# Performance work log

Measured on AMD Instinct MI355X. Metric: run time of the kernel, lower is better.

The kernel has to match this reference:

```python
import jax, jax.numpy as jnp
import numpy as np

IN_FEAT, H_FEAT, NUM_CLASSES = 7, 8, 2
N_NODES, N_EDGES, N_GRAPHS = 40000, 640000, 64
DIMS = [IN_FEAT, H_FEAT, H_FEAT * 2, H_FEAT * 4, H_FEAT * 8, H_FEAT * 16]  # 7,8,16,32,64,128


def setup_inputs() -> dict:
    key = jax.random.key(0)
    ks = jax.random.split(key, 20)
    inp = {
        "x": jax.random.normal(ks[0], (N_NODES, IN_FEAT), dtype=jnp.float32),
        "edge_index": jax.random.randint(ks[1], (2, N_EDGES), 0, N_NODES, dtype=jnp.int32),
        "edge_attr": jax.random.uniform(ks[2], (N_EDGES,), dtype=jnp.float32),
        "batch": jnp.sort(jax.random.randint(ks[3], (N_NODES,), 0, N_GRAPHS, dtype=jnp.int32)),
    }
    # GraphConv params: lin_rel (with bias) applied to aggregated messages,
    # lin_root (no bias) applied to x itself. Stored as [in, out]; y = x @ W.
    for i in range(5):
        fi, fo = DIMS[i], DIMS[i + 1]
        s = 1.0 / np.sqrt(fi)
        inp[f"w_rel{i+1}"] = jax.random.uniform(ks[4 + 3 * i], (fi, fo), minval=-s, maxval=s, dtype=jnp.float32)
        inp[f"b_rel{i+1}"] = jax.random.uniform(ks[5 + 3 * i], (fo,), minval=-s, maxval=s, dtype=jnp.float32)
        inp[f"w_root{i+1}"] = jax.random.uniform(ks[6 + 3 * i], (fi, fo), minval=-s, maxval=s, dtype=jnp.float32)
    s = 1.0 / np.sqrt(DIMS[-1])
    inp["w_lin"] = jax.random.uniform(ks[19], (DIMS[-1], NUM_CLASSES), minval=-s, maxval=s, dtype=jnp.float32)
    inp["b_lin"] = jax.random.uniform(jax.random.fold_in(key, 99), (NUM_CLASSES,), minval=-s, maxval=s, dtype=jnp.float32)
    return inp


def graph_conv(x, src, dst, ew, w_rel, b_rel, w_root):
    # message: edge_weight * x[src]; aggregate by sum at dst (PyG GraphConv, aggr='add')
    msg = x[src] * ew[:, None]                               # [E, Fin]
    agg = jax.ops.segment_sum(msg, dst, num_segments=N_NODES)  # [N, Fin]
    return agg @ w_rel + b_rel + x @ w_root                  # [N, Fout]


def reference(x, edge_index, edge_attr, batch,
              w_rel1, b_rel1, w_root1, w_rel2, b_rel2, w_root2,
              w_rel3, b_rel3, w_root3, w_rel4, b_rel4, w_root4,
              w_rel5, b_rel5, w_root5, w_lin, b_lin):
    src, dst = edge_index[0], edge_index[1]
    h = x
    params = [(w_rel1, b_rel1, w_root1), (w_rel2, b_rel2, w_root2),
              (w_rel3, b_rel3, w_root3), (w_rel4, b_rel4, w_root4),
              (w_rel5, b_rel5, w_root5)]
    for wr, br, wo in params:
        h = graph_conv(h, src, dst, edge_attr, wr, br, wo)
    pooled = jax.ops.segment_sum(h, batch, num_segments=N_GRAPHS)  # [G, 128]
    return pooled @ w_lin + b_lin                                  # [G, 2]
```

## Files before the change

### kernel.cpp

```cpp
#include <hip/hip_runtime.h>

#define N_NODES 40000
#define N_EDGES 640000
#define N_GRAPHS 64

typedef unsigned short u16;
typedef unsigned int u32;
typedef __attribute__((ext_vector_type(8))) short bf16x8;
typedef __attribute__((ext_vector_type(4))) float f32x4;

static inline int cdiv(long long a, int b) { return (int)((a + b - 1) / b); }

__device__ __forceinline__ u16 f2bf(float f) {
    u32 u = __float_as_uint(f);
    u32 r = (u + 0x7fffu + ((u >> 16) & 1u)) >> 16;
    return (u16)r;
}
__device__ __forceinline__ u32 packpair(float a, float b) {
    return (u32)f2bf(a) | ((u32)f2bf(b) << 16);
}
__device__ __forceinline__ void unpack8(uint4 q, float* o) {
    o[0] = __uint_as_float(q.x << 16); o[1] = __uint_as_float(q.x & 0xffff0000u);
    o[2] = __uint_as_float(q.y << 16); o[3] = __uint_as_float(q.y & 0xffff0000u);
    o[4] = __uint_as_float(q.z << 16); o[5] = __uint_as_float(q.z & 0xffff0000u);
    o[6] = __uint_as_float(q.w << 16); o[7] = __uint_as_float(q.w & 0xffff0000u);
}

__device__ __forceinline__ void pack_one(int idx, int KS, int Kreal, int FOUT,
                                         const float* __restrict__ wrel,
                                         const float* __restrict__ wroot,
                                         u16* __restrict__ out) {
    int j = idx & 7;
    int lane = (idx >> 3) & 63;
    int rest = idx >> 9;
    int nt = rest / KS, ks = rest - nt * KS;
    int k = ks * 32 + (lane >> 4) * 8 + j;
    int col = nt * 16 + (lane & 15);
    float v = 0.f;
    if (k < Kreal / 2) v = wrel[k * FOUT + col];
    else if (k < Kreal) v = wroot[(k - Kreal / 2) * FOUT + col];
    out[idx] = f2bf(v);
}

__global__ __launch_bounds__(256) void prep_kernel(
        const float* __restrict__ x, u16* __restrict__ xbf,
        const float* __restrict__ wr2, const float* __restrict__ wo2,
        const float* __restrict__ wr3, const float* __restrict__ wo3,
        const float* __restrict__ wr4, const float* __restrict__ wo4,
        const float* __restrict__ wr5, const float* __restrict__ wo5,
        u16* __restrict__ p2, u16* __restrict__ p3,
        u16* __restrict__ p4, u16* __restrict__ p5,
        int* __restrict__ deg, float* __restrict__ pooled) {
    int tid = blockIdx.x * 256 + threadIdx.x;
    if (tid < 40000) {
        int n = tid;
        float v[8];
        #pragma unroll
        for (int i = 0; i < 7; ++i) v[i] = x[n * 7 + i];
        v[7] = 0.f;
        uint4 q;
        q.x = packpair(v[0], v[1]); q.y = packpair(v[2], v[3]);
        q.z = packpair(v[4], v[5]); q.w = packpair(v[6], v[7]);
        *(uint4*)(xbf + (long long)n * 8) = q;
    } else if (tid < 62016) {
        int t = tid - 40000;
        if (t < 512)        pack_one(t,        1,  16,  16,  wr2, wo2, p2);
        else if (t < 1536)  pack_one(t - 512,  1,  32,  32,  wr3, wo3, p3);
        else if (t < 5632)  pack_one(t - 1536, 2,  64,  64,  wr4, wo4, p4);
        else                pack_one(t - 5632, 4, 128, 128,  wr5, wo5, p5);
    } else if (tid < 102016) {
        deg[tid - 62016] = 0;
    } else if (tid < 110208) {
        pooled[tid - 102016] = 0.f;
    }
}

__global__ __launch_bounds__(256) void hist_kernel(const int* __restrict__ dst,
                                                   int* __restrict__ deg) {
    int e = blockIdx.x * 256 + threadIdx.x;
    if (e < N_EDGES) atomicAdd(&deg[dst[e]], 1);
}

__global__ __launch_bounds__(1024) void scan_part(const int* __restrict__ deg,
                                                  int* __restrict__ row_start,
                                                  int* __restrict__ bsum) {
    __shared__ int wtot[16], woff[16];
    int tid = threadIdx.x;
    int i = blockIdx.x * 1024 + tid;
    int v = (i < N_NODES) ? deg[i] : 0;
    int lane = tid & 63, wid = tid >> 6;
    int inc = v;
    #pragma unroll
    for (int off = 1; off < 64; off <<= 1) {
        int y = __shfl_up(inc, off, 64);
        if (lane >= off) inc += y;
    }
    if (lane == 63) wtot[wid] = inc;
    __syncthreads();
    if (tid < 16) {
        int b = wtot[tid];
        #pragma unroll
        for (int off = 1; off < 16; off <<= 1) {
            int y = __shfl_up(b, off, 16);
            if ((tid & 15) >= off) b += y;
        }
        woff[tid] = b - wtot[tid];
        if (tid == 15) bsum[blockIdx.x] = b;
    }
    __syncthreads();
    if (i <= N_NODES) row_start[i] = woff[wid] + inc - v;
}

__global__ __launch_bounds__(1024) void scan_add(int* __restrict__ row_start,
                                                 const int* __restrict__ bsum,
                                                 int* __restrict__ cursor) {
    __shared__ int sbase;
    int tid = threadIdx.x;
    if (tid < 64) {
        int b = (tid < blockIdx.x) ? bsum[tid] : 0;
        #pragma unroll
        for (int off = 32; off; off >>= 1) b += __shfl_xor(b, off, 64);
        if (tid == 0) sbase = b;
    }
    __syncthreads();
    int i = blockIdx.x * 1024 + tid;
    if (i <= N_NODES) {
        int v = row_start[i] + sbase;
        row_start[i] = v;
        if (i < N_NODES) cursor[i] = v;
    }
}

__global__ __launch_bounds__(256) void scatter_kernel(const int* __restrict__ src,
                                                      const int* __restrict__ dst,
                                                      const float* __restrict__ ew,
                                                      int* __restrict__ cursor,
                                                      int2* __restrict__ csr_pair) {
    int e = blockIdx.x * 256 + threadIdx.x;
    if (e >= N_EDGES) return;
    int pos = atomicAdd(&cursor[dst[e]], 1);
    int2 q;
    q.x = src[e];
    q.y = __float_as_int(ew[e]);
    csr_pair[pos] = q;
}

template<int LOGF, int SLOG>
__global__ __launch_bounds__(256) void gather_bf16(const u16* __restrict__ hin,
                                                   const int* __restrict__ rs,
                                                   const int2* __restrict__ pair,
                                                   u16* __restrict__ agg) {
    constexpr int FIN = 8 << LOGF;
    constexpr int S = 1 << SLOG;
    long long tid = (long long)blockIdx.x * 256 + threadIdx.x;
    int n = (int)(tid >> (LOGF + SLOG));
    if (n >= N_NODES) return;
    int sub = (int)(tid & ((1 << (LOGF + SLOG)) - 1));
    int c = sub & ((1 << LOGF) - 1);
    int half = sub >> LOGF;
    const u16* base = hin + c * 8;
    int beg = rs[n], end = rs[n + 1];
    float acc[8] = {0.f, 0.f, 0.f, 0.f, 0.f, 0.f, 0.f, 0.f};
    int p = beg + half;
    int s = 0; float w = 0.f;
    if (p < end) { int2 q = pair[p]; s = q.x; w = __int_as_float(q.y); }
    while (p < end) {
        uint4 rq = *(const uint4*)(base + (long long)s * FIN);
        float wc = w;
        int pn = p + S;
        if (pn < end) { int2 q = pair[pn]; s = q.x; w = __int_as_float(q.y); }
        float tv[8];
        unpack8(rq, tv);
        #pragma unroll
        for (int j = 0; j < 8; ++j) acc[j] = fmaf(wc, tv[j], acc[j]);
        p = pn;
    }
    #pragma unroll
    for (int d = (1 << LOGF); d < (1 << (LOGF + SLOG)); d <<= 1) {
        #pragma unroll
        for (int j = 0; j < 8; ++j) acc[j] += __shfl_xor(acc[j], d, 64);
    }
    if (half == 0) {
        uint4 o;
        o.x = packpair(acc[0], acc[1]); o.y = packpair(acc[2], acc[3]);
        o.z = packpair(acc[4], acc[5]); o.w = packpair(acc[6], acc[7]);
        *(uint4*)(agg + (long long)n * FIN + c * 8) = o;
    }
}

__global__ __launch_bounds__(256) void node1b(const u16* __restrict__ agg1,
                                              const u16* __restrict__ xbf,
                                              const float* __restrict__ wr,
                                              const float* __restrict__ br,
                                              const float* __restrict__ wo,
                                              u16* __restrict__ h2) {
    __shared__ float swr[56], swo[56], sb[8];
    if (threadIdx.x < 56) { swr[threadIdx.x] = wr[threadIdx.x]; swo[threadIdx.x] = wo[threadIdx.x]; }
    if (threadIdx.x < 8) sb[threadIdx.x] = br[threadIdx.x];
    __syncthreads();
    int n = blockIdx.x * 256 + threadIdx.x;
    if (n >= N_NODES) return;
    float a[8], h[8];
    uint4 qa = *(const uint4*)(agg1 + (long long)n * 8);
    uint4 qh = *(const uint4*)(xbf + (long long)n * 8);
    unpack8(qa, a);
    unpack8(qh, h);
    float o[8];
    #pragma unroll
    for (int j = 0; j < 8; ++j) {
        float s = sb[j];
        #pragma unroll
        for (int i = 0; i < 7; ++i) s = fmaf(a[i], swr[i * 8 + j], fmaf(h[i], swo[i * 8 + j], s));
        o[j] = s;
    }
    uint4 q;
    q.x = packpair(o[0], o[1]); q.y = packpair(o[2], o[3]);
    q.z = packpair(o[4], o[5]); q.w = packpair(o[6], o[7]);
    *(uint4*)(h2 + (long long)n * 8) = q;
}

template<int FIN, int FOUT, bool POOL>
__global__ __launch_bounds__(64) void node_mfma(const u16* __restrict__ agg,
                                                const u16* __restrict__ hin,
                                                const u16* __restrict__ bpack,
                                                const float* __restrict__ b_rel,
                                                u16* __restrict__ hout,
                                                const int* __restrict__ batch,
                                                float* __restrict__ pooled) {
    constexpr int KREAL = 2 * FIN;
    constexpr int K = (KREAL < 32) ? 32 : KREAL;
    constexpr int KS = K / 32;
    constexpr int NT = FOUT / 16;
    int lane = threadIdx.x;
    int tile = blockIdx.x;
    int col = lane & 15;
    int node_a = tile * 16 + col;
    int kgrp = (lane >> 4) * 8;

    f32x4 acc[NT];
    #pragma unroll
    for (int nt = 0; nt < NT; ++nt) {
        float bv = b_rel[nt * 16 + col];
        acc[nt] = (f32x4){bv, bv, bv, bv};
    }

    #pragma unroll
    for (int ks = 0; ks < KS; ++ks) {
        int k0 = ks * 32 + kgrp;
        bf16x8 af;
        if (k0 < FIN)
            af = *(const bf16x8*)(agg + (long long)node_a * FIN + k0);
        else if (k0 < KREAL)
            af = *(const bf16x8*)(hin + (long long)node_a * FIN + (k0 - FIN));
        else
            af = (bf16x8)(short)0;
        #pragma unroll
        for (int nt = 0; nt < NT; ++nt) {
            bf16x8 bf = *(const bf16x8*)(bpack + (((nt * KS + ks) << 6) + lane) * 8);
            acc[nt] = __builtin_amdgcn_mfma_f32_16x16x32_bf16(af, bf, acc[nt], 0, 0, 0);
        }
    }

    int row0 = tile * 16 + (lane >> 4) * 4;
    if constexpr (!POOL) {
        #pragma unroll
        for (int nt = 0; nt < NT; ++nt)
            #pragma unroll
            for (int r = 0; r < 4; ++r)
                hout[(long long)(row0 + r) * FOUT + nt * 16 + col] = f2bf(acc[nt][r]);
    } else {
        int b_first = batch[tile * 16];
        int b_last = batch[tile * 16 + 15];
        if (b_first == b_last) {
            #pragma unroll
            for (int nt = 0; nt < NT; ++nt) {
                float s = acc[nt][0] + acc[nt][1] + acc[nt][2] + acc[nt][3];
                s += __shfl_xor(s, 16, 64);
                s += __shfl_xor(s, 32, 64);
                if (lane < 16) atomicAdd(&pooled[b_first * FOUT + nt * 16 + col], s);
            }
        } else {
            #pragma unroll
            for (int r = 0; r < 4; ++r) {
                int g = batch[row0 + r];
                #pragma unroll
                for (int nt = 0; nt < NT; ++nt)
                    atomicAdd(&pooled[g * FOUT + nt * 16 + col], acc[nt][r]);
            }
        }
    }
}

__global__ void final_kernel(const float* __restrict__ pooled,
                             const float* __restrict__ w_lin,
                             const float* __restrict__ b_lin,
                             float* __restrict__ out) {
    int tid = threadIdx.x;
    int g = tid >> 1;
    int c = tid & 1;
    float acc = b_lin[c];
    #pragma unroll 8
    for (int fi = 0; fi < 128; ++fi)
        acc += pooled[g * 128 + fi] * w_lin[fi * 2 + c];
    out[g * 2 + c] = acc;
}

extern "C" void kernel_launch(void* const* d_in, const int* in_sizes, int n_in,
                              void* d_out, int out_size, void* d_ws, size_t ws_size,
                              hipStream_t stream) {
    const float* x     = (const float*)d_in[0];
    const int*   ei    = (const int*)d_in[1];
    const float* ea    = (const float*)d_in[2];
    const int*   batch = (const int*)d_in[3];
    const int* src = ei;
    const int* dst = ei + N_EDGES;

    const float* w_rel[5], *b_rel[5], *w_root[5];
    for (int i = 0; i < 5; ++i) {
        w_rel[i]  = (const float*)d_in[4 + 3 * i];
        b_rel[i]  = (const float*)d_in[5 + 3 * i];
        w_root[i] = (const float*)d_in[6 + 3 * i];
    }
    const float* w_lin = (const float*)d_in[19];
    const float* b_lin = (const float*)d_in[20];
    float* out = (float*)d_out;

    u16*   xbf     = (u16*)d_ws;
    u16*   agg     = xbf + 320000;
    u16*   h2      = agg + 2560000;
    u16*   h3      = h2 + 320000;
    u16*   h4      = h3 + 640000;
    u16*   h5      = h4 + 1280000;
    float* pooled  = (float*)(h5 + 2560000);
    u16*   p2      = (u16*)(pooled + N_GRAPHS * 128);
    u16*   p3      = p2 + 512;
    u16*   p4      = p3 + 1024;
    u16*   p5      = p4 + 4096;
    int2*  csr_pair= (int2*)(p5 + 16384);
    int*   deg     = (int*)(csr_pair + N_EDGES);
    int*   rs      = deg + N_NODES;
    int*   cursor  = rs + N_NODES + 1;
    int*   bsum    = cursor + N_NODES;

    const int BLK = 256;
    const int EB = cdiv(N_EDGES, BLK);

    prep_kernel<<<431, BLK, 0, stream>>>(x, xbf,
                                         w_rel[1], w_root[1], w_rel[2], w_root[2],
                                         w_rel[3], w_root[3], w_rel[4], w_root[4],
                                         p2, p3, p4, p5, deg, pooled);
    hist_kernel<<<EB, BLK, 0, stream>>>(dst, deg);
    scan_part<<<40, 1024, 0, stream>>>(deg, rs, bsum);
    scan_add<<<40, 1024, 0, stream>>>(rs, bsum, cursor);
    scatter_kernel<<<EB, BLK, 0, stream>>>(src, dst, ea, cursor, csr_pair);

    gather_bf16<0, 3><<<cdiv((long long)N_NODES * 8, BLK), BLK, 0, stream>>>(
        xbf, rs, csr_pair, agg);
    node1b<<<cdiv(N_NODES, BLK), BLK, 0, stream>>>(agg, xbf, w_rel[0], b_rel[0], w_root[0], h2);

    gather_bf16<0, 3><<<cdiv((long long)N_NODES * 8, BLK), BLK, 0, stream>>>(
        h2, rs, csr_pair, agg);
    node_mfma<8, 16, false><<<2500, 64, 0, stream>>>(agg, h2, p2, b_rel[1], h3, nullptr, nullptr);

    gather_bf16<1, 3><<<cdiv((long long)N_NODES * 16, BLK), BLK, 0, stream>>>(
        h3, rs, csr_pair, agg);
    node_mfma<16, 32, false><<<2500, 64, 0, stream>>>(agg, h3, p3, b_rel[2], h4, nullptr, nullptr);

    gather_bf16<2, 3><<<cdiv((long long)N_NODES * 32, BLK), BLK, 0, stream>>>(
        h4, rs, csr_pair, agg);
    node_mfma<32, 64, false><<<2500, 64, 0, stream>>>(agg, h4, p4, b_rel[3], h5, nullptr, nullptr);

    gather_bf16<3, 3><<<cdiv((long long)N_NODES * 64, BLK), BLK, 0, stream>>>(
        h5, rs, csr_pair, agg);
    node_mfma<64, 128, true><<<2500, 64, 0, stream>>>(agg, h5, p5, b_rel[4], nullptr, batch, pooled);

    final_kernel<<<1, 128, 0, stream>>>(pooled, w_lin, b_lin, out);
}
```

Measured before the change: 240.8 us.

## Fuse neighbor gather with dense transform per layer via LDS staging

Merges each layer's CSR gather into the MFMA node-transform kernel, staging the 16-node aggregate tile in shared memory instead of writing and rereading a global agg buffer. Layer 1's gather is also fused with its scalar transform, with each of 8 lanes producing one output feature. This removes kernel launches and global traffic for the aggregate. The cost is 1024-thread blocks with one wave per node, which leaves many lanes idle for narrow layers, and only NT waves doing MFMA after the barrier.

```diff
diff --git a/kernel.cpp b/kernel.cpp
--- a/kernel.cpp
+++ b/kernel.cpp
@@ -145,29 +145,30 @@
     csr_pair[pos] = q;
 }
 
-template<int LOGF, int SLOG>
-__global__ __launch_bounds__(256) void gather_bf16(const u16* __restrict__ hin,
-                                                   const int* __restrict__ rs,
-                                                   const int2* __restrict__ pair,
-                                                   u16* __restrict__ agg) {
-    constexpr int FIN = 8 << LOGF;
-    constexpr int S = 1 << SLOG;
-    long long tid = (long long)blockIdx.x * 256 + threadIdx.x;
-    int n = (int)(tid >> (LOGF + SLOG));
+__global__ __launch_bounds__(256) void gather_node1(const u16* __restrict__ xbf,
+                                                    const int* __restrict__ rs,
+                                                    const int2* __restrict__ pair,
+                                                    const float* __restrict__ wr,
+                                                    const float* __restrict__ br,
+                                                    const float* __restrict__ wo,
+                                                    u16* __restrict__ h2) {
+    __shared__ float swr[56], swo[56], sb[8];
+    if (threadIdx.x < 56) { swr[threadIdx.x] = wr[threadIdx.x]; swo[threadIdx.x] = wo[threadIdx.x]; }
+    if (threadIdx.x < 8) sb[threadIdx.x] = br[threadIdx.x];
+    __syncthreads();
+    int tid = blockIdx.x * 256 + threadIdx.x;
+    int n = tid >> 3;
     if (n >= N_NODES) return;
-    int sub = (int)(tid & ((1 << (LOGF + SLOG)) - 1));
-    int c = sub & ((1 << LOGF) - 1);
-    int half = sub >> LOGF;
-    const u16* base = hin + c * 8;
+    int s3 = tid & 7;
     int beg = rs[n], end = rs[n + 1];
     float acc[8] = {0.f, 0.f, 0.f, 0.f, 0.f, 0.f, 0.f, 0.f};
-    int p = beg + half;
+    int p = beg + s3;
     int s = 0; float w = 0.f;
     if (p < end) { int2 q = pair[p]; s = q.x; w = __int_as_float(q.y); }
     while (p < end) {
-        uint4 rq = *(const uint4*)(base + (long long)s * FIN);
+        uint4 rq = *(const uint4*)(xbf + (long long)s * 8);
         float wc = w;
-        int pn = p + S;
+        int pn = p + 8;
         if (pn < end) { int2 q = pair[pn]; s = q.x; w = __int_as_float(q.y); }
         float tv[8];
         unpack8(rq, tv);
@@ -176,116 +177,119 @@
         p = pn;
     }
     #pragma unroll
-    for (int d = (1 << LOGF); d < (1 << (LOGF + SLOG)); d <<= 1) {
+    for (int d = 1; d < 8; d <<= 1) {
         #pragma unroll
         for (int j = 0; j < 8; ++j) acc[j] += __shfl_xor(acc[j], d, 64);
     }
-    if (half == 0) {
-        uint4 o;
-        o.x = packpair(acc[0], acc[1]); o.y = packpair(acc[2], acc[3]);
-        o.z = packpair(acc[4], acc[5]); o.w = packpair(acc[6], acc[7]);
-        *(uint4*)(agg + (long long)n * FIN + c * 8) = o;
-    }
-}
-
-__global__ __launch_bounds__(256) void node1b(const u16* __restrict__ agg1,
-                                              const u16* __restrict__ xbf,
-                                              const float* __restrict__ wr,
-                                              const float* __restrict__ br,
-                                              const float* __restrict__ wo,
-                                              u16* __restrict__ h2) {
-    __shared__ float swr[56], swo[56], sb[8];
-    if (threadIdx.x < 56) { swr[threadIdx.x] = wr[threadIdx.x]; swo[threadIdx.x] = wo[threadIdx.x]; }
-    if (threadIdx.x < 8) sb[threadIdx.x] = br[threadIdx.x];
-    __syncthreads();
-    int n = blockIdx.x * 256 + threadIdx.x;
-    if (n >= N_NODES) return;
-    float a[8], h[8];
-    uint4 qa = *(const uint4*)(agg1 + (long long)n * 8);
     uint4 qh = *(const uint4*)(xbf + (long long)n * 8);
-    unpack8(qa, a);
+    float h[8];
     unpack8(qh, h);
-    float o[8];
+    float o = sb[s3];
     #pragma unroll
-    for (int j = 0; j < 8; ++j) {
-        float s = sb[j];
-        #pragma unroll
-        for (int i = 0; i < 7; ++i) s = fmaf(a[i], swr[i * 8 + j], fmaf(h[i], swo[i * 8 + j], s));
-        o[j] = s;
-    }
-    uint4 q;
-    q.x = packpair(o[0], o[1]); q.y = packpair(o[2], o[3]);
-    q.z = packpair(o[4], o[5]); q.w = packpair(o[6], o[7]);
-    *(uint4*)(h2 + (long long)n * 8) = q;
-}
-
-template<int FIN, int FOUT, bool POOL>
-__global__ __launch_bounds__(64) void node_mfma(const u16* __restrict__ agg,
-                                                const u16* __restrict__ hin,
-                                                const u16* __restrict__ bpack,
-                                                const float* __restrict__ b_rel,
-                                                u16* __restrict__ hout,
-                                                const int* __restrict__ batch,
-                                                float* __restrict__ pooled) {
+    for (int i = 0; i < 7; ++i)
+        o = fmaf(acc[i], swr[i * 8 + s3], fmaf(h[i], swo[i * 8 + s3], o));
+    h2[(long long)n * 8 + s3] = f2bf(o);
+}
+
+template<int LOGC, int FOUT, bool POOL>
+__global__ __launch_bounds__(1024) void fused_layer(const u16* __restrict__ hin,
+                                                    const int* __restrict__ rs,
+                                                    const int2* __restrict__ pair,
+                                                    const u16* __restrict__ bpack,
+                                                    const float* __restrict__ b_rel,
+                                                    u16* __restrict__ hout,
+                                                    const int* __restrict__ batch,
+                                                    float* __restrict__ pooled) {
+    constexpr int FIN = 8 << LOGC;
     constexpr int KREAL = 2 * FIN;
     constexpr int K = (KREAL < 32) ? 32 : KREAL;
     constexpr int KS = K / 32;
     constexpr int NT = FOUT / 16;
-    int lane = threadIdx.x;
-    int tile = blockIdx.x;
+    constexpr int CHUNKS = 1 << LOGC;
+    constexpr int SPLIT = 64 >> LOGC;
+    constexpr int LDK = FIN + 8;
+
+    __shared__ u16 lds[16][LDK];
+
+    int tid = threadIdx.x;
+    int wave = tid >> 6;
+    int lane = tid & 63;
+    int node0 = blockIdx.x * 16;
+
+    {
+        int n = node0 + wave;
+        int beg = rs[n], end = rs[n + 1];
+        int c = lane & (CHUNKS - 1);
+        int half = lane >> LOGC;
+        float acc[8] = {0.f, 0.f, 0.f, 0.f, 0.f, 0.f, 0.f, 0.f};
+        int p = beg + half;
+        int s = 0; float w = 0.f;
+        if (p < end) { int2 q = pair[p]; s = q.x; w = __int_as_float(q.y); }
+        while (p < end) {
+            uint4 rq = *(const uint4*)(hin + (long long)s * FIN + c * 8);
+            float wc = w;
+            int pn = p + SPLIT;
+            if (pn < end) { int2 q = pair[pn]; s = q.x; w = __int_as_float(q.y); }
+            float tv[8];
+            unpack8(rq, tv);
+            #pragma unroll
+            for (int j = 0; j < 8; ++j) acc[j] = fmaf(wc, tv[j], acc[j]);
+            p = pn;
+        }
+        #pragma unroll
+        for (int d = CHUNKS; d < 64; d <<= 1) {
+            #pragma unroll
+            for (int j = 0; j < 8; ++j) acc[j] += __shfl_xor(acc[j], d, 64);
+        }
+        if (half == 0) {
+            uint4 o;
+            o.x = packpair(acc[0], acc[1]); o.y = packpair(acc[2], acc[3]);
+            o.z = packpair(acc[4], acc[5]); o.w = packpair(acc[6], acc[7]);
+            *(uint4*)&lds[wave][c * 8] = o;
+        }
+    }
+    __syncthreads();
+
+    if (wave >= NT) return;
+    int nt = wave;
     int col = lane & 15;
-    int node_a = tile * 16 + col;
     int kgrp = (lane >> 4) * 8;
 
-    f32x4 acc[NT];
-    #pragma unroll
-    for (int nt = 0; nt < NT; ++nt) {
-        float bv = b_rel[nt * 16 + col];
-        acc[nt] = (f32x4){bv, bv, bv, bv};
-    }
+    float bv = b_rel[nt * 16 + col];
+    f32x4 acc4 = (f32x4){bv, bv, bv, bv};
 
     #pragma unroll
     for (int ks = 0; ks < KS; ++ks) {
         int k0 = ks * 32 + kgrp;
         bf16x8 af;
         if (k0 < FIN)
-            af = *(const bf16x8*)(agg + (long long)node_a * FIN + k0);
+            af = *(const bf16x8*)&lds[col][k0];
         else if (k0 < KREAL)
-            af = *(const bf16x8*)(hin + (long long)node_a * FIN + (k0 - FIN));
+            af = *(const bf16x8*)(hin + (long long)(node0 + col) * FIN + (k0 - FIN));
         else
             af = (bf16x8)(short)0;
-        #pragma unroll
-        for (int nt = 0; nt < NT; ++nt) {
-            bf16x8 bf = *(const bf16x8*)(bpack + (((nt * KS + ks) << 6) + lane) * 8);
-            acc[nt] = __builtin_amdgcn_mfma_f32_16x16x32_bf16(af, bf, acc[nt], 0, 0, 0);
-        }
-    }
-
-    int row0 = tile * 16 + (lane >> 4) * 4;
+        bf16x8 bf = *(const bf16x8*)(bpack + (((nt * KS + ks) << 6) + lane) * 8);
+        acc4 = __builtin_amdgcn_mfma_f32_16x16x32_bf16(af, bf, acc4, 0, 0, 0);
+    }
+
+    int row0 = (lane >> 4) * 4;
     if constexpr (!POOL) {
         #pragma unroll
-        for (int nt = 0; nt < NT; ++nt)
-            #pragma unroll
-            for (int r = 0; r < 4; ++r)
-                hout[(long long)(row0 + r) * FOUT + nt * 16 + col] = f2bf(acc[nt][r]);
+        for (int r = 0; r < 4; ++r)
+            hout[(long long)(node0 + row0 + r) * FOUT + nt * 16 + col] = f2bf(acc4[r]);
     } else {
-        int b_first = batch[tile * 16];
-        int b_last = batch[tile * 16 + 15];
+        int b_first = batch[node0];
+        int b_last = batch[node0 + 15];
         if (b_first == b_last) {
-            #pragma unroll
-            for (int nt = 0; nt < NT; ++nt) {
-                float s = acc[nt][0] + acc[nt][1] + acc[nt][2] + acc[nt][3];
-                s += __shfl_xor(s, 16, 64);
-                s += __shfl_xor(s, 32, 64);
-                if (lane < 16) atomicAdd(&pooled[b_first * FOUT + nt * 16 + col], s);
-            }
+            float s = acc4[0] + acc4[1] + acc4[2] + acc4[3];
+            s += __shfl_xor(s, 16, 64);
+            s += __shfl_xor(s, 32, 64);
+            if (lane < 16) atomicAdd(&pooled[b_first * FOUT + nt * 16 + col], s);
         } else {
             #pragma unroll
             for (int r = 0; r < 4; ++r) {
-                int g = batch[row0 + r];
-                #pragma unroll
-                for (int nt = 0; nt < NT; ++nt)
-                    atomicAdd(&pooled[g * FOUT + nt * 16 + col], acc[nt][r]);
+                int g = batch[node0 + row0 + r];
+                atomicAdd(&pooled[g * FOUT + nt * 16 + col], acc4[r]);
             }
         }
     }
@@ -326,8 +330,7 @@
     float* out = (float*)d_out;
 
     u16*   xbf     = (u16*)d_ws;
-    u16*   agg     = xbf + 320000;
-    u16*   h2      = agg + 2560000;
+    u16*   h2      = xbf + 320000;
     u16*   h3      = h2 + 320000;
     u16*   h4      = h3 + 640000;
     u16*   h5      = h4 + 1280000;
@@ -354,25 +357,12 @@
     scan_add<<<40, 1024, 0, stream>>>(rs, bsum, cursor);
     scatter_kernel<<<EB, BLK, 0, stream>>>(src, dst, ea, cursor, csr_pair);
 
-    gather_bf16<0, 3><<<cdiv((long long)N_NODES * 8, BLK), BLK, 0, stream>>>(
-        xbf, rs, csr_pair, agg);
-    node1b<<<cdiv(N_NODES, BLK), BLK, 0, stream>>>(agg, xbf, w_rel[0], b_rel[0], w_root[0], h2);
-
-    gather_bf16<0, 3><<<cdiv((long long)N_NODES * 8, BLK), BLK, 0, stream>>>(
-        h2, rs, csr_pair, agg);
-    node_mfma<8, 16, false><<<2500, 64, 0, stream>>>(agg, h2, p2, b_rel[1], h3, nullptr, nullptr);
-
-    gather_bf16<1, 3><<<cdiv((long long)N_NODES * 16, BLK), BLK, 0, stream>>>(
-        h3, rs, csr_pair, agg);
-    node_mfma<16, 32, false><<<2500, 64, 0, stream>>>(agg, h3, p3, b_rel[2], h4, nullptr, nullptr);
-
-    gather_bf16<2, 3><<<cdiv((long long)N_NODES * 32, BLK), BLK, 0, stream>>>(
-        h4, rs, csr_pair, agg);
-    node_mfma<32, 64, false><<<2500, 64, 0, stream>>>(agg, h4, p4, b_rel[3], h5, nullptr, nullptr);
-
-    gather_bf16<3, 3><<<cdiv((long long)N_NODES * 64, BLK), BLK, 0, stream>>>(
-        h5, rs, csr_pair, agg);
-    node_mfma<64, 128, true><<<2500, 64, 0, stream>>>(agg, h5, p5, b_rel[4], nullptr, batch, pooled);
+    gather_node1<<<1250, BLK, 0, stream>>>(xbf, rs, csr_pair, w_rel[0], b_rel[0], w_root[0], h2);
+
+    fused_layer<0, 16, false><<<2500, 1024, 0, stream>>>(h2, rs, csr_pair, p2, b_rel[1], h3, nullptr, nullptr);
+    fused_layer<1, 32, false><<<2500, 1024, 0, stream>>>(h3, rs, csr_pair, p3, b_rel[2], h4, nullptr, nullptr);
+    fused_layer<2, 64, false><<<2500, 1024, 0, stream>>>(h4, rs, csr_pair, p4, b_rel[3], h5, nullptr, nullptr);
+    fused_layer<3, 128, true><<<2500, 1024, 0, stream>>>(h5, rs, csr_pair, p5, b_rel[4], nullptr, batch, pooled);
 
     final_kernel<<<1, 128, 0, stream>>>(pooled, w_lin, b_lin, out);
 }
```

New measurement: 269.5 us. 1.12x slower.

## Fold last GraphConv layer and pooling into per-graph edge sums with precomputed weights

Applied to the files above, without the earlier changes.

Since the last layer is linear and followed by sum pooling and a linear head, the layer-5 gather and MFMA are replaced by direct per-graph accumulation of edge-weighted h5[src] (grouped by batch[dst]) and of h5 per node, plus node counts. These sums are then combined with precomputed products W_rel5·W_lin, W_root5·W_lin and b_rel5·W_lin in the final kernel. Separately, the first gather and node1b are fused into one kernel. This removes the widest gather and GEMM layer, at the cost of LDS atomic contention in edge_pool and a different fp32 summation order.

```diff
diff --git a/kernel.cpp b/kernel.cpp
--- a/kernel.cpp
+++ b/kernel.cpp
@@ -48,9 +48,10 @@
         const float* __restrict__ wr3, const float* __restrict__ wo3,
         const float* __restrict__ wr4, const float* __restrict__ wo4,
         const float* __restrict__ wr5, const float* __restrict__ wo5,
-        u16* __restrict__ p2, u16* __restrict__ p3,
-        u16* __restrict__ p4, u16* __restrict__ p5,
-        int* __restrict__ deg, float* __restrict__ pooled) {
+        const float* __restrict__ br5, const float* __restrict__ w_lin,
+        u16* __restrict__ p2, u16* __restrict__ p3, u16* __restrict__ p4,
+        int* __restrict__ deg, float* __restrict__ Szero,
+        float* __restrict__ M, float* __restrict__ bb) {
     int tid = blockIdx.x * 256 + threadIdx.x;
     if (tid < 40000) {
         int n = tid;
@@ -62,16 +63,27 @@
         q.x = packpair(v[0], v[1]); q.y = packpair(v[2], v[3]);
         q.z = packpair(v[4], v[5]); q.w = packpair(v[6], v[7]);
         *(uint4*)(xbf + (long long)n * 8) = q;
-    } else if (tid < 62016) {
+    } else if (tid < 45632) {
         int t = tid - 40000;
-        if (t < 512)        pack_one(t,        1,  16,  16,  wr2, wo2, p2);
-        else if (t < 1536)  pack_one(t - 512,  1,  32,  32,  wr3, wo3, p3);
-        else if (t < 5632)  pack_one(t - 1536, 2,  64,  64,  wr4, wo4, p4);
-        else                pack_one(t - 5632, 4, 128, 128,  wr5, wo5, p5);
-    } else if (tid < 102016) {
-        deg[tid - 62016] = 0;
-    } else if (tid < 110208) {
-        pooled[tid - 102016] = 0.f;
+        if (t < 512)        pack_one(t,        1, 16, 16, wr2, wo2, p2);
+        else if (t < 1536)  pack_one(t - 512,  1, 32, 32, wr3, wo3, p3);
+        else                pack_one(t - 1536, 2, 64, 64, wr4, wo4, p4);
+    } else if (tid < 85632) {
+        deg[tid - 45632] = 0;
+    } else if (tid < 93888) {
+        Szero[tid - 85632] = 0.f;
+    } else if (tid < 94144) {
+        int t = tid - 93888;
+        int k = t >> 1, c = t & 1;
+        const float* wk = (k < 64) ? (wr5 + k * 128) : (wo5 + (k - 64) * 128);
+        float a = 0.f;
+        for (int j = 0; j < 128; ++j) a += wk[j] * w_lin[j * 2 + c];
+        M[t] = a;
+    } else if (tid < 94146) {
+        int c = tid - 94144;
+        float a = 0.f;
+        for (int j = 0; j < 128; ++j) a += br5[j] * w_lin[j * 2 + c];
+        bb[c] = a;
     }
 }
 
@@ -143,6 +155,52 @@
     q.x = src[e];
     q.y = __float_as_int(ew[e]);
     csr_pair[pos] = q;
+}
+
+__global__ __launch_bounds__(256) void gather_node1(const u16* __restrict__ xbf,
+                                                    const int* __restrict__ rs,
+                                                    const int2* __restrict__ pair,
+                                                    const float* __restrict__ wr,
+                                                    const float* __restrict__ br,
+                                                    const float* __restrict__ wo,
+                                                    u16* __restrict__ h2) {
+    __shared__ float swr[56], swo[56], sb[8];
+    if (threadIdx.x < 56) { swr[threadIdx.x] = wr[threadIdx.x]; swo[threadIdx.x] = wo[threadIdx.x]; }
+    if (threadIdx.x < 8) sb[threadIdx.x] = br[threadIdx.x];
+    __syncthreads();
+    int tid = blockIdx.x * 256 + threadIdx.x;
+    int n = tid >> 3;
+    if (n >= N_NODES) return;
+    int s3 = tid & 7;
+    int beg = rs[n], end = rs[n + 1];
+    float acc[8] = {0.f, 0.f, 0.f, 0.f, 0.f, 0.f, 0.f, 0.f};
+    int p = beg + s3;
+    int s = 0; float w = 0.f;
+    if (p < end) { int2 q = pair[p]; s = q.x; w = __int_as_float(q.y); }
+    while (p < end) {
+        uint4 rq = *(const uint4*)(xbf + (long long)s * 8);
+        float wc = w;
+        int pn = p + 8;
+        if (pn < end) { int2 q = pair[pn]; s = q.x; w = __int_as_float(q.y); }
+        float tv[8];
+        unpack8(rq, tv);
+        #pragma unroll
+        for (int j = 0; j < 8; ++j) acc[j] = fmaf(wc, tv[j], acc[j]);
+        p = pn;
+    }
+    #pragma unroll
+    for (int d = 1; d < 8; d <<= 1) {
+        #pragma unroll
+        for (int j = 0; j < 8; ++j) acc[j] += __shfl_xor(acc[j], d, 64);
+    }
+    uint4 qh = *(const uint4*)(xbf + (long long)n * 8);
+    float h[8];
+    unpack8(qh, h);
+    float o = sb[s3];
+    #pragma unroll
+    for (int i = 0; i < 7; ++i)
+        o = fmaf(acc[i], swr[i * 8 + s3], fmaf(h[i], swo[i * 8 + s3], o));
+    h2[(long long)n * 8 + s3] = f2bf(o);
 }
 
 template<int LOGF, int SLOG>
@@ -188,45 +246,12 @@
     }
 }
 
-__global__ __launch_bounds__(256) void node1b(const u16* __restrict__ agg1,
-                                              const u16* __restrict__ xbf,
-                                              const float* __restrict__ wr,
-                                              const float* __restrict__ br,
-                                              const float* __restrict__ wo,
-                                              u16* __restrict__ h2) {
-    __shared__ float swr[56], swo[56], sb[8];
-    if (threadIdx.x < 56) { swr[threadIdx.x] = wr[threadIdx.x]; swo[threadIdx.x] = wo[threadIdx.x]; }
-    if (threadIdx.x < 8) sb[threadIdx.x] = br[threadIdx.x];
-    __syncthreads();
-    int n = blockIdx.x * 256 + threadIdx.x;
-    if (n >= N_NODES) return;
-    float a[8], h[8];
-    uint4 qa = *(const uint4*)(agg1 + (long long)n * 8);
-    uint4 qh = *(const uint4*)(xbf + (long long)n * 8);
-    unpack8(qa, a);
-    unpack8(qh, h);
-    float o[8];
-    #pragma unroll
-    for (int j = 0; j < 8; ++j) {
-        float s = sb[j];
-        #pragma unroll
-        for (int i = 0; i < 7; ++i) s = fmaf(a[i], swr[i * 8 + j], fmaf(h[i], swo[i * 8 + j], s));
-        o[j] = s;
-    }
-    uint4 q;
-    q.x = packpair(o[0], o[1]); q.y = packpair(o[2], o[3]);
-    q.z = packpair(o[4], o[5]); q.w = packpair(o[6], o[7]);
-    *(uint4*)(h2 + (long long)n * 8) = q;
-}
-
-template<int FIN, int FOUT, bool POOL>
+template<int FIN, int FOUT>
 __global__ __launch_bounds__(64) void node_mfma(const u16* __restrict__ agg,
                                                 const u16* __restrict__ hin,
                                                 const u16* __restrict__ bpack,
                                                 const float* __restrict__ b_rel,
-                                                u16* __restrict__ hout,
-                                                const int* __restrict__ batch,
-                                                float* __restrict__ pooled) {
+                                                u16* __restrict__ hout) {
     constexpr int KREAL = 2 * FIN;
     constexpr int K = (KREAL < 32) ? 32 : KREAL;
     constexpr int KS = K / 32;
@@ -262,46 +287,82 @@
     }
 
     int row0 = tile * 16 + (lane >> 4) * 4;
-    if constexpr (!POOL) {
-        #pragma unroll
-        for (int nt = 0; nt < NT; ++nt)
-            #pragma unroll
-            for (int r = 0; r < 4; ++r)
-                hout[(long long)(row0 + r) * FOUT + nt * 16 + col] = f2bf(acc[nt][r]);
+    #pragma unroll
+    for (int nt = 0; nt < NT; ++nt)
+        #pragma unroll
+        for (int r = 0; r < 4; ++r)
+            hout[(long long)(row0 + r) * FOUT + nt * 16 + col] = f2bf(acc[nt][r]);
+}
+
+__global__ __launch_bounds__(256) void edge_pool(const u16* __restrict__ h5,
+                                                 const int* __restrict__ src,
+                                                 const int* __restrict__ dst,
+                                                 const float* __restrict__ ea,
+                                                 const int* __restrict__ batch,
+                                                 float* __restrict__ S_rel,
+                                                 float* __restrict__ S_root,
+                                                 float* __restrict__ cnt) {
+    __shared__ float acc[4096];
+    __shared__ float cacc[64];
+    int tid = threadIdx.x;
+    int wv = tid >> 6, lane = tid & 63;
+    for (int i = tid; i < 4096; i += 256) acc[i] = 0.f;
+    if (tid < 64) cacc[tid] = 0.f;
+    __syncthreads();
+
+    bool isEdge = blockIdx.x < 512;
+    if (isEdge) {
+        int base = blockIdx.x * 1250;
+        int e0 = base + wv * 313;
+        int e1 = base + 1250; if (e0 + 313 < e1) e1 = e0 + 313;
+        #pragma unroll 4
+        for (int e = e0; e < e1; ++e) {
+            int s = src[e];
+            int g = batch[dst[e]];
+            float w = ea[e];
+            float v = __uint_as_float((u32)h5[(long long)s * 64 + lane] << 16);
+            atomicAdd(&acc[g * 64 + lane], w * v);
+        }
     } else {
-        int b_first = batch[tile * 16];
-        int b_last = batch[tile * 16 + 15];
-        if (b_first == b_last) {
-            #pragma unroll
-            for (int nt = 0; nt < NT; ++nt) {
-                float s = acc[nt][0] + acc[nt][1] + acc[nt][2] + acc[nt][3];
-                s += __shfl_xor(s, 16, 64);
-                s += __shfl_xor(s, 32, 64);
-                if (lane < 16) atomicAdd(&pooled[b_first * FOUT + nt * 16 + col], s);
-            }
-        } else {
-            #pragma unroll
-            for (int r = 0; r < 4; ++r) {
-                int g = batch[row0 + r];
-                #pragma unroll
-                for (int nt = 0; nt < NT; ++nt)
-                    atomicAdd(&pooled[g * FOUT + nt * 16 + col], acc[nt][r]);
-            }
+        int base = (blockIdx.x - 512) * 1250;
+        int n0 = base + wv * 313;
+        int n1 = base + 1250; if (n0 + 313 < n1) n1 = n0 + 313;
+        for (int n = n0; n < n1; ++n) {
+            int g = batch[n];
+            float v = __uint_as_float((u32)h5[(long long)n * 64 + lane] << 16);
+            atomicAdd(&acc[g * 64 + lane], v);
+            if (lane == 0) atomicAdd(&cacc[g], 1.f);
         }
     }
-}
-
-__global__ void final_kernel(const float* __restrict__ pooled,
-                             const float* __restrict__ w_lin,
+    __syncthreads();
+
+    float* Sout = isEdge ? S_rel : S_root;
+    for (int i = tid; i < 4096; i += 256) {
+        float v = acc[i];
+        if (v != 0.f) atomicAdd(&Sout[i], v);
+    }
+    if (!isEdge && tid < 64) {
+        float c2 = cacc[tid];
+        if (c2 != 0.f) atomicAdd(&cnt[tid], c2);
+    }
+}
+
+__global__ void final_kernel(const float* __restrict__ S_rel,
+                             const float* __restrict__ S_root,
+                             const float* __restrict__ cnt,
+                             const float* __restrict__ M,
+                             const float* __restrict__ bb,
                              const float* __restrict__ b_lin,
                              float* __restrict__ out) {
     int tid = threadIdx.x;
     int g = tid >> 1;
     int c = tid & 1;
-    float acc = b_lin[c];
+    float acc = b_lin[c] + cnt[g] * bb[c];
     #pragma unroll 8
-    for (int fi = 0; fi < 128; ++fi)
-        acc += pooled[g * 128 + fi] * w_lin[fi * 2 + c];
+    for (int k = 0; k < 64; ++k) {
+        acc += S_rel[g * 64 + k] * M[k * 2 + c];
+        acc += S_root[g * 64 + k] * M[(64 + k) * 2 + c];
+    }
     out[g * 2 + c] = acc;
 }
 
@@ -327,16 +388,19 @@
 
     u16*   xbf     = (u16*)d_ws;
     u16*   agg     = xbf + 320000;
-    u16*   h2      = agg + 2560000;
+    u16*   h2      = agg + 1280000;
     u16*   h3      = h2 + 320000;
     u16*   h4      = h3 + 640000;
     u16*   h5      = h4 + 1280000;
-    float* pooled  = (float*)(h5 + 2560000);
-    u16*   p2      = (u16*)(pooled + N_GRAPHS * 128);
+    u16*   p2      = h5 + 2560000;
     u16*   p3      = p2 + 512;
     u16*   p4      = p3 + 1024;
-    u16*   p5      = p4 + 4096;
-    int2*  csr_pair= (int2*)(p5 + 16384);
+    float* S_rel   = (float*)(p4 + 4096);
+    float* S_root  = S_rel + 4096;
+    float* cnt     = S_root + 4096;
+    float* M       = cnt + 64;
+    float* bb      = M + 256;
+    int2*  csr_pair= (int2*)(bb + 4);
     int*   deg     = (int*)(csr_pair + N_EDGES);
     int*   rs      = deg + N_NODES;
     int*   cursor  = rs + N_NODES + 1;
@@ -345,34 +409,31 @@
     const int BLK = 256;
     const int EB = cdiv(N_EDGES, BLK);
 
-    prep_kernel<<<431, BLK, 0, stream>>>(x, xbf,
+    prep_kernel<<<368, BLK, 0, stream>>>(x, xbf,
                                          w_rel[1], w_root[1], w_rel[2], w_root[2],
                                          w_rel[3], w_root[3], w_rel[4], w_root[4],
-                                         p2, p3, p4, p5, deg, pooled);
+                                         b_rel[4], w_lin,
+                                         p2, p3, p4, deg, S_rel, M, bb);
     hist_kernel<<<EB, BLK, 0, stream>>>(dst, deg);
     scan_part<<<40, 1024, 0, stream>>>(deg, rs, bsum);
     scan_add<<<40, 1024, 0, stream>>>(rs, bsum, cursor);
     scatter_kernel<<<EB, BLK, 0, stream>>>(src, dst, ea, cursor, csr_pair);
 
-    gather_bf16<0, 3><<<cdiv((long long)N_NODES * 8, BLK), BLK, 0, stream>>>(
-        xbf, rs, csr_pair, agg);
-    node1b<<<cdiv(N_NODES, BLK), BLK, 0, stream>>>(agg, xbf, w_rel[0], b_rel[0], w_root[0], h2);
+    gather_node1<<<1250, BLK, 0, stream>>>(xbf, rs, csr_pair, w_rel[0], b_rel[0], w_root[0], h2);
 
     gather_bf16<0, 3><<<cdiv((long long)N_NODES * 8, BLK), BLK, 0, stream>>>(
         h2, rs, csr_pair, agg);
-    node_mfma<8, 16, false><<<2500, 64, 0, stream>>>(agg, h2, p2, b_rel[1], h3, nullptr, nullptr);
+    node_mfma<8, 16><<<2500, 64, 0, stream>>>(agg, h2, p2, b_rel[1], h3);
 
     gather_bf16<1, 3><<<cdiv((long long)N_NODES * 16, BLK), BLK, 0, stream>>>(
         h3, rs, csr_pair, agg);
-    node_mfma<16, 32, false><<<2500, 64, 0, stream>>>(agg, h3, p3, b_rel[2], h4, nullptr, nullptr);
+    node_mfma<16, 32><<<2500, 64, 0, stream>>>(agg, h3, p3, b_rel[2], h4);
 
     gather_bf16<2, 3><<<cdiv((long long)N_NODES * 32, BLK), BLK, 0, stream>>>(
         h4, rs, csr_pair, agg);
-    node_mfma<32, 64, false><<<2500, 64, 0, stream>>>(agg, h4, p4, b_rel[3], h5, nullptr, nullptr);
-
-    gather_bf16<3, 3><<<cdiv((long long)N_NODES * 64, BLK), BLK, 0, stream>>>(
-        h5, rs, csr_pair, agg);
-    node_mfma<64, 128, true><<<2500, 64, 0, stream>>>(agg, h5, p5, b_rel[4], nullptr, batch, pooled);
-
-    final_kernel<<<1, 128, 0, stream>>>(pooled, w_lin, b_lin, out);
-}
+    node_mfma<32, 64><<<2500, 64, 0, stream>>>(agg, h4, p4, b_rel[3], h5);
+
+    edge_pool<<<544, BLK, 0, stream>>>(h5, src, dst, ea, batch, S_rel, S_root, cnt);
+
+    final_kernel<<<1, 128, 0, stream>>>(S_rel, S_root, cnt, M, bb, b_lin, out);
+}
```

Measured after the change: 525.5 us. 2.18x slower.
